# Performance work log

Measured on AMD Instinct MI355X. Metric: run time of the kernel, lower is better.

## Reference

```python
import jax, jax.numpy as jnp
import numpy as np

B, T, D = 64, 512, 256   # batch, time, input feat
H = 256                  # LSTM hidden (features)


def setup_inputs() -> dict:
    key = jax.random.key(0)
    ks = jax.random.split(key, 16)
    s = lambda k, shp, fan: jax.random.normal(k, shp, jnp.float32) / np.sqrt(fan)
    return {
        "x":  jax.random.normal(ks[0], (B, T, D), jnp.float32),
        # LSTM params: fused gates order (i, f, g, o)
        "Wi": s(ks[1], (D, 4 * H), D),
        "Wh": s(ks[2], (H, 4 * H), H),
        "b":  jnp.zeros((4 * H,), jnp.float32),
        # single-head attention (head_dim = H)
        "Wq": s(ks[3], (H, H), H), "bq": jnp.zeros((H,), jnp.float32),
        "Wk": s(ks[4], (H, H), H), "bk": jnp.zeros((H,), jnp.float32),
        "Wv": s(ks[5], (H, H), H), "bv": jnp.zeros((H,), jnp.float32),
        "Wo": s(ks[6], (H, H), H), "bo": jnp.zeros((H,), jnp.float32),
        # MLP head
        "W1": s(ks[7], (H, 32), H), "b1": jnp.zeros((32,), jnp.float32),
        "W2": s(ks[8], (32, 3), 32), "b2": jnp.zeros((3,), jnp.float32),
    }


def _lstm_scan(x, Wi, Wh, b):
    # Precompute input-to-hidden projection for all timesteps (batched GEMM)
    xg = jnp.einsum('btd,dg->btg', x, Wi) + b          # [B,T,4H]
    c0 = jnp.zeros((x.shape[0], Wh.shape[0]), x.dtype)
    h0 = jnp.zeros_like(c0)

    def step(carry, xg_t):
        c, h = carry
        g = xg_t + h @ Wh                               # [B,4H]
        i, f, gg, o = jnp.split(g, 4, axis=-1)          # flax gate order i,f,g,o
        c = jax.nn.sigmoid(f) * c + jax.nn.sigmoid(i) * jnp.tanh(gg)
        h = jax.nn.sigmoid(o) * jnp.tanh(c)
        return (c, h), h

    (_, _), hs = jax.lax.scan(step, (c0, h0), jnp.swapaxes(xg, 0, 1))
    return jnp.swapaxes(hs, 0, 1)                       # [B,T,H]


def reference(x, Wi, Wh, b, Wq, bq, Wk, bk, Wv, bv, Wo, bo, W1, b1, W2, b2):
    h = _lstm_scan(x, Wi, Wh, b)                        # [B,T,H]
    # single-head dot-product attention (self-attention)
    q = h @ Wq + bq
    k = h @ Wk + bk
    v = h @ Wv + bv
    scale = 1.0 / np.sqrt(q.shape[-1]).astype(np.float32)
    scores = jnp.einsum('bqd,bkd->bqk', q * scale, k)   # [B,T,T]
    attn = jax.nn.softmax(scores, axis=-1)
    o = jnp.einsum('bqk,bkd->bqd', attn, v)
    o = o @ Wo + bo                                     # output projection
    # head on first timestep
    z = jax.nn.relu(o[:, 0, :] @ W1 + b1)
    return z @ W2 + b2                                  # [B,3]
```

## Files before the change

### kernel.cpp

```cpp
#include <hip/hip_runtime.h>
#include <hip/hip_bf16.h>


typedef __attribute__((ext_vector_type(8))) short short8;
typedef __attribute__((ext_vector_type(4))) float float4v;

__device__ __forceinline__ unsigned short f2bf(float f) {
  unsigned u = __builtin_bit_cast(unsigned, f);
  return (unsigned short)((u + 0x7fffu + ((u >> 16) & 1u)) >> 16);
}
__device__ __forceinline__ float bf2f(unsigned short h) {
  return __builtin_bit_cast(float, ((unsigned)h) << 16);
}
__device__ __forceinline__ float bcl(unsigned u) {
  return __builtin_bit_cast(float, u << 16);
}
__device__ __forceinline__ float bch(unsigned u) {
  return __builtin_bit_cast(float, u & 0xffff0000u);
}
__device__ __forceinline__ float sigm(float x) { return 1.f / (1.f + __expf(-x)); }
__device__ __forceinline__ float tanh_f(float x) { return 1.f - 2.f / (1.f + __expf(2.f * x)); }

__global__ void prep_x(const float* __restrict__ x, unsigned short* __restrict__ xbf) {
  size_t i = ((size_t)blockIdx.x * 256 + threadIdx.x) * 4;
  float4 v = *(const float4*)&x[i];
  unsigned long long pk = (unsigned long long)f2bf(v.x)
                        | ((unsigned long long)f2bf(v.y) << 16)
                        | ((unsigned long long)f2bf(v.z) << 32)
                        | ((unsigned long long)f2bf(v.w) << 48);
  *(unsigned long long*)&xbf[i] = pk;
}

__global__ void prep_wit(const float* __restrict__ Wi, unsigned short* __restrict__ WiT) {
  size_t i = ((size_t)blockIdx.x * 256 + threadIdx.x) * 4;
  float4 v = *(const float4*)&Wi[i];
  int k = (int)(i >> 10), n = (int)(i & 1023);
  WiT[(size_t)(n + 0) * 256 + k] = f2bf(v.x);
  WiT[(size_t)(n + 1) * 256 + k] = f2bf(v.y);
  WiT[(size_t)(n + 2) * 256 + k] = f2bf(v.z);
  WiT[(size_t)(n + 3) * 256 + k] = f2bf(v.w);
}

__global__ void init_hx(unsigned long long* __restrict__ hx) {
  hx[(size_t)blockIdx.x * 256 + threadIdx.x] = 0xffffffff00000000ULL;
}

#define XKP 40
__global__ __launch_bounds__(256) void xg_gemm(const unsigned short* __restrict__ xbf,
                                               const unsigned short* __restrict__ WiT,
                                               const float* __restrict__ bias,
                                               unsigned short* __restrict__ xg) {
  __shared__ unsigned short As[128 * XKP];
  __shared__ unsigned short Bs[128 * XKP];
  const int tid = threadIdx.x;
  const int n0 = blockIdx.x * 128, m0 = blockIdx.y * 128;
  const int wave = tid >> 6, lane = tid & 63, quad = lane >> 4, l16 = lane & 15;
  const int wm = wave >> 1, wn = wave & 1;

  float4v acc[4][4];
#pragma unroll
  for (int i = 0; i < 4; ++i)
#pragma unroll
    for (int j = 0; j < 4; ++j) acc[i][j] = (float4v){0.f, 0.f, 0.f, 0.f};

  const int rr = tid >> 2, c8 = (tid & 3) * 8;
  for (int k0 = 0; k0 < 256; k0 += 32) {
#pragma unroll
    for (int pp = 0; pp < 2; ++pp) {
      int r = pp * 64 + rr;
      *(uint4*)&As[r * XKP + c8] = *(const uint4*)&xbf[(size_t)(m0 + r) * 256 + k0 + c8];
      *(uint4*)&Bs[r * XKP + c8] = *(const uint4*)&WiT[(size_t)(n0 + r) * 256 + k0 + c8];
    }
    __syncthreads();
#pragma unroll
    for (int mt = 0; mt < 4; ++mt) {
      short8 af = *(const short8*)&As[(wm * 64 + mt * 16 + l16) * XKP + quad * 8];
#pragma unroll
      for (int nt = 0; nt < 4; ++nt) {
        short8 bf = *(const short8*)&Bs[(wn * 64 + nt * 16 + l16) * XKP + quad * 8];
        acc[mt][nt] = __builtin_amdgcn_mfma_f32_16x16x32_bf16(af, bf, acc[mt][nt], 0, 0, 0);
      }
    }
    __syncthreads();
  }
#pragma unroll
  for (int nt = 0; nt < 4; ++nt) {
    int col = n0 + wn * 64 + nt * 16 + l16;
    int gate = col >> 8, ggx = (col >> 4) & 15, ul = col & 15;
    float bv = bias[col];
#pragma unroll
    for (int mt = 0; mt < 4; ++mt) {
#pragma unroll
      for (int r = 0; r < 4; ++r) {
        int row = m0 + wm * 64 + mt * 16 + quad * 4 + r;
        int b = row >> 9, t = row & 511;
        xg[(((size_t)ggx * 64 + b) * 512 + t) * 64 + gate * 16 + ul] =
            f2bf(acc[mt][nt][r] + bv);
      }
    }
  }
}

#define KP2 264
__global__ __launch_bounds__(256) void lstm_scan(const float* __restrict__ Wh,
                                                 const unsigned short* __restrict__ xgbuf,
                                                 unsigned short* __restrict__ hout,
                                                 unsigned long long* __restrict__ hx) {
  __shared__ unsigned short WhS[64 * KP2];
  __shared__ unsigned short hA[16 * KP2];
  __shared__ float preS[16 * 68];
  __shared__ float cS[256];
  const int tid = threadIdx.x;
  const int wg = blockIdx.x, bg = wg >> 4, gg = wg & 15;
  const int wave = tid >> 6, lane = tid & 63, quad = lane >> 4, l16 = lane & 15;

  {
    int uu = tid & 15, kh = tid >> 4;
#pragma unroll
    for (int gt = 0; gt < 4; ++gt)
      for (int kb = 0; kb < 16; ++kb) {
        int k = kb * 16 + kh;
        WhS[(gt * 16 + uu) * KP2 + k] = f2bf(Wh[(size_t)k * 1024 + gt * 256 + gg * 16 + uu]);
      }
  }
  for (int i = tid; i < 16 * KP2; i += 256) hA[i] = 0;
  cS[tid] = 0.f;
  __syncthreads();

  const int b_loc = tid >> 4, u_loc = tid & 15;
  const int bgb = bg * 16 + b_loc;
  const int u_glob = gg * 16 + u_loc;
  const int nrow = wave * 16 + l16;
  const unsigned short* xgp0 = xgbuf + ((size_t)(gg * 64 + bgb) * 512) * 64 + u_loc;

  unsigned short xi = xgp0[0], xf = xgp0[16], xG = xgp0[32], xo = xgp0[48];

  for (int t = 0; t < 512; ++t) {
    float4v acc = (float4v){0.f, 0.f, 0.f, 0.f};
#pragma unroll
    for (int kt = 0; kt < 8; ++kt) {
      short8 af = *(const short8*)&hA[l16 * KP2 + kt * 32 + quad * 8];
      short8 bf = *(const short8*)&WhS[nrow * KP2 + kt * 32 + quad * 8];
      acc = __builtin_amdgcn_mfma_f32_16x16x32_bf16(af, bf, acc, 0, 0, 0);
    }
#pragma unroll
    for (int r = 0; r < 4; ++r)
      preS[(quad * 4 + r) * 68 + wave * 16 + l16] = acc[r];

    int tn = (t < 511) ? t + 1 : t;
    const unsigned short* xgn = xgp0 + (size_t)tn * 64;
    unsigned short nxi = xgn[0], nxf = xgn[16], nxG = xgn[32], nxo = xgn[48];
    __syncthreads();

    float gi = preS[b_loc * 68 + 0 * 16 + u_loc] + bf2f(xi);
    float gf = preS[b_loc * 68 + 1 * 16 + u_loc] + bf2f(xf);
    float gG = preS[b_loc * 68 + 2 * 16 + u_loc] + bf2f(xG);
    float go = preS[b_loc * 68 + 3 * 16 + u_loc] + bf2f(xo);
    float c = sigm(gf) * cS[tid] + sigm(gi) * tanh_f(gG);
    cS[tid] = c;
    float h = sigm(go) * tanh_f(c);
    unsigned hb = (unsigned)f2bf(h);
    hA[b_loc * KP2 + u_glob] = (unsigned short)hb;

    const unsigned tg = (unsigned)t;
    unsigned v1 = __shfl_down((int)hb, 1);
    if ((u_loc & 1) == 0) {
      unsigned d0 = hb | (v1 << 16);
      unsigned long long val = (unsigned long long)d0 | ((unsigned long long)tg << 32);
      unsigned long long* dst =
          hx + (((size_t)(t & 1) * 64 + bgb) * 128 + (u_glob >> 1));
      __hip_atomic_store(dst, val, __ATOMIC_RELAXED, __HIP_MEMORY_SCOPE_AGENT);
      *(unsigned*)&hout[((size_t)bgb * 512 + t) * 256 + u_glob] = d0;
    }

    {
      int b2 = tid >> 4, grp = tid & 15;
      if (grp != gg) {
        const unsigned long long* base =
            hx + (((size_t)(t & 1) * 64 + bg * 16 + b2) * 128 + grp * 8);
        unsigned long long w[8];
        int guard = 0;
        bool ok;
        do {
          ok = true;
#pragma unroll
          for (int i = 0; i < 8; ++i) {
            w[i] = __hip_atomic_load(&base[i], __ATOMIC_RELAXED,
                                     __HIP_MEMORY_SCOPE_AGENT);
            ok &= ((unsigned)(w[i] >> 32) == tg);
          }
        } while (!ok && ++guard < (1 << 20));
        int u0 = grp * 16;
#pragma unroll
        for (int i = 0; i < 8; ++i)
          *(unsigned*)&hA[b2 * KP2 + u0 + 2 * i] = (unsigned)w[i];
      }
    }
    xi = nxi; xf = nxf; xG = nxG; xo = nxo;
    __syncthreads();
  }
}

__global__ __launch_bounds__(256) void attn_qu(const unsigned short* __restrict__ hout,
                                               const float* __restrict__ Wq,
                                               const float* __restrict__ bq,
                                               const float* __restrict__ Wk,
                                               const float* __restrict__ bk,
                                               float* __restrict__ us,
                                               float* __restrict__ cbuf) {
  __shared__ float h0S[256], q0S[256], red[256];
  const int b = blockIdx.x, tid = threadIdx.x;
  h0S[tid] = bf2f(hout[(size_t)b * 512 * 256 + tid]);
  __syncthreads();
  float a = 0.f;
  for (int k = 0; k < 256; ++k) a += h0S[k] * Wq[(size_t)k * 256 + tid];
  q0S[tid] = a + bq[tid];
  __syncthreads();
  red[tid] = q0S[tid] * bk[tid];
  __syncthreads();
  for (int s = 128; s > 0; s >>= 1) {
    if (tid < s) red[tid] += red[tid + s];
    __syncthreads();
  }
  if (tid == 0) cbuf[b] = 0.0625f * red[0];
  float acc = 0.f;
  const float* wr = &Wk[(size_t)tid * 256];
  for (int e = 0; e < 256; e += 4) {
    float4 w = *(const float4*)&wr[e];
    acc += w.x * q0S[e] + w.y * q0S[e + 1] + w.z * q0S[e + 2] + w.w * q0S[e + 3];
  }
  us[b * 256 + tid] = 0.0625f * acc;
}

__global__ __launch_bounds__(256) void attn_sm(const unsigned short* __restrict__ hout,
                                               const float* __restrict__ us,
                                               const float* __restrict__ cbuf,
                                               float* __restrict__ hbar) {
  __shared__ float sS[512], red[256], hb4[4][256];
  const int b = blockIdx.x, tid = threadIdx.x, wave = tid >> 6, lane = tid & 63;
  const size_t hb_base = (size_t)b * 512 * 256;
  const float u0 = us[b * 256 + lane * 4 + 0], u1 = us[b * 256 + lane * 4 + 1];
  const float u2 = us[b * 256 + lane * 4 + 2], u3 = us[b * 256 + lane * 4 + 3];
  const float cbv = cbuf[b];
  for (int i = 0; i < 128; ++i) {
    int t = i * 4 + wave;
    unsigned long long hv = *(const unsigned long long*)&hout[hb_base + (size_t)t * 256 + lane * 4];
    unsigned lo = (unsigned)hv, hi = (unsigned)(hv >> 32);
    float p = u0 * bcl(lo) + u1 * bch(lo) + u2 * bcl(hi) + u3 * bch(hi);
    for (int m = 1; m < 64; m <<= 1) p += __shfl_xor(p, m, 64);
    if (lane == 0) sS[t] = p + cbv;
  }
  __syncthreads();
  red[tid] = fmaxf(sS[tid], sS[tid + 256]);
  __syncthreads();
  for (int s = 128; s > 0; s >>= 1) {
    if (tid < s) red[tid] = fmaxf(red[tid], red[tid + s]);
    __syncthreads();
  }
  float mx = red[0];
  __syncthreads();
  float e0 = __expf(sS[tid] - mx), e1 = __expf(sS[tid + 256] - mx);
  sS[tid] = e0; sS[tid + 256] = e1;
  red[tid] = e0 + e1;
  __syncthreads();
  for (int s = 128; s > 0; s >>= 1) {
    if (tid < s) red[tid] += red[tid + s];
    __syncthreads();
  }
  float inv = 1.f / red[0];
  float a0 = 0.f, a1 = 0.f, a2 = 0.f, a3 = 0.f;
  const int d0 = lane * 4;
  for (int i = 0; i < 128; ++i) {
    int t = wave * 128 + i;
    float w = sS[t];
    unsigned long long hv = *(const unsigned long long*)&hout[hb_base + (size_t)t * 256 + d0];
    unsigned lo = (unsigned)hv, hi = (unsigned)(hv >> 32);
    a0 += w * bcl(lo); a1 += w * bch(lo); a2 += w * bcl(hi); a3 += w * bch(hi);
  }
  hb4[wave][d0] = a0; hb4[wave][d0 + 1] = a1; hb4[wave][d0 + 2] = a2; hb4[wave][d0 + 3] = a3;
  __syncthreads();
  hbar[b * 256 + tid] = (hb4[0][tid] + hb4[1][tid] + hb4[2][tid] + hb4[3][tid]) * inv;
}

__global__ __launch_bounds__(256) void head_k(const float* __restrict__ hbar,
                                              const float* __restrict__ Wv, const float* __restrict__ bv,
                                              const float* __restrict__ Wo, const float* __restrict__ bo,
                                              const float* __restrict__ W1, const float* __restrict__ b1,
                                              const float* __restrict__ W2, const float* __restrict__ b2,
                                              float* __restrict__ out) {
  __shared__ float hS[256], oS[256], o1S[256], zS[32];
  const int b = blockIdx.x, tid = threadIdx.x;
  hS[tid] = hbar[b * 256 + tid];
  __syncthreads();
  float a = 0.f;
  for (int k = 0; k < 256; ++k) a += hS[k] * Wv[(size_t)k * 256 + tid];
  oS[tid] = a + bv[tid];
  __syncthreads();
  a = 0.f;
  for (int k = 0; k < 256; ++k) a += oS[k] * Wo[(size_t)k * 256 + tid];
  o1S[tid] = a + bo[tid];
  __syncthreads();
  if (tid < 32) {
    a = 0.f;
    for (int k = 0; k < 256; ++k) a += o1S[k] * W1[k * 32 + tid];
    zS[tid] = fmaxf(a + b1[tid], 0.f);
  }
  __syncthreads();
  if (tid < 3) {
    a = 0.f;
    for (int j = 0; j < 32; ++j) a += zS[j] * W2[j * 3 + tid];
    out[b * 3 + tid] = a + b2[tid];
  }
}

extern "C" void kernel_launch(void* const* d_in, const int* in_sizes, int n_in,
                              void* d_out, int out_size, void* d_ws, size_t ws_size,
                              hipStream_t stream) {
  const float* x  = (const float*)d_in[0];
  const float* Wi = (const float*)d_in[1];
  const float* Wh = (const float*)d_in[2];
  const float* bG = (const float*)d_in[3];
  const float* Wq = (const float*)d_in[4];
  const float* bq = (const float*)d_in[5];
  const float* Wk = (const float*)d_in[6];
  const float* bk = (const float*)d_in[7];
  const float* Wv = (const float*)d_in[8];
  const float* bv = (const float*)d_in[9];
  const float* Wo = (const float*)d_in[10];
  const float* bo = (const float*)d_in[11];
  const float* W1 = (const float*)d_in[12];
  const float* b1 = (const float*)d_in[13];
  const float* W2 = (const float*)d_in[14];
  const float* b2 = (const float*)d_in[15];
  float* out = (float*)d_out;
  char* ws = (char*)d_ws;

  unsigned short* xg    = (unsigned short*)(ws);
  unsigned short* hout  = (unsigned short*)(ws + 67108864);
  unsigned short* xbf   = (unsigned short*)(ws + 83886080);
  unsigned short* WiT   = (unsigned short*)(ws + 100663296);
  unsigned long long* hx = (unsigned long long*)(ws + 101187584);
  float*          us    = (float*)(ws + 101318656);
  float*          cbuf  = (float*)(ws + 101384192);
  float*          hbar  = (float*)(ws + 101385216);

  prep_x<<<dim3(8192), dim3(256), 0, stream>>>(x, xbf);
  prep_wit<<<dim3(256), dim3(256), 0, stream>>>(Wi, WiT);
  init_hx<<<dim3(64), dim3(256), 0, stream>>>(hx);
  xg_gemm<<<dim3(8, 256), dim3(256), 0, stream>>>(xbf, WiT, bG, xg);
  lstm_scan<<<dim3(64), dim3(256), 0, stream>>>(Wh, xg, hout, hx);
  attn_qu<<<dim3(64), dim3(256), 0, stream>>>(hout, Wq, bq, Wk, bk, us, cbuf);
  attn_sm<<<dim3(64), dim3(256), 0, stream>>>(hout, us, cbuf, hbar);
  head_k<<<dim3(64), dim3(256), 0, stream>>>(hbar, Wv, bv, Wo, bo, W1, b1, W2, b2, out);
}
```

Baseline: 1.406 ms.

## Run LSTM scan one batch row per block with register-resident Wh, fuse kernels

The LSTM recurrence is restructured so each block owns a single batch row and all 1024 gate columns. Most of the bf16 Wh is held as MFMA fragments in registers and the rest in swizzled LDS. This replaces the cross-block atomic flag exchange of h between 16 column-group blocks with plain block-level barriers. The xg layout is changed so each unit's four gates are contiguous. Prep kernels are merged into one, which also pre-permutes Wh. The attention kernels and head are fused into one kernel, and the activations use hardware reciprocals. In exchange, each block now runs a 16-wide MFMA with only one valid batch column, so most of the matrix work is wasted. Register pressure also rises with 48 short8 fragments per lane.

```diff
diff --git a/kernel.cpp b/kernel.cpp
--- a/kernel.cpp
+++ b/kernel.cpp
@@ -18,31 +18,49 @@
 __device__ __forceinline__ float bch(unsigned u) {
   return __builtin_bit_cast(float, u & 0xffff0000u);
 }
-__device__ __forceinline__ float sigm(float x) { return 1.f / (1.f + __expf(-x)); }
-__device__ __forceinline__ float tanh_f(float x) { return 1.f - 2.f / (1.f + __expf(2.f * x)); }
-
-__global__ void prep_x(const float* __restrict__ x, unsigned short* __restrict__ xbf) {
-  size_t i = ((size_t)blockIdx.x * 256 + threadIdx.x) * 4;
-  float4 v = *(const float4*)&x[i];
-  unsigned long long pk = (unsigned long long)f2bf(v.x)
-                        | ((unsigned long long)f2bf(v.y) << 16)
-                        | ((unsigned long long)f2bf(v.z) << 32)
-                        | ((unsigned long long)f2bf(v.w) << 48);
-  *(unsigned long long*)&xbf[i] = pk;
-}
-
-__global__ void prep_wit(const float* __restrict__ Wi, unsigned short* __restrict__ WiT) {
-  size_t i = ((size_t)blockIdx.x * 256 + threadIdx.x) * 4;
-  float4 v = *(const float4*)&Wi[i];
-  int k = (int)(i >> 10), n = (int)(i & 1023);
-  WiT[(size_t)(n + 0) * 256 + k] = f2bf(v.x);
-  WiT[(size_t)(n + 1) * 256 + k] = f2bf(v.y);
-  WiT[(size_t)(n + 2) * 256 + k] = f2bf(v.z);
-  WiT[(size_t)(n + 3) * 256 + k] = f2bf(v.w);
-}
-
-__global__ void init_hx(unsigned long long* __restrict__ hx) {
-  hx[(size_t)blockIdx.x * 256 + threadIdx.x] = 0xffffffff00000000ULL;
+__device__ __forceinline__ float sigm(float x) {
+  return __builtin_amdgcn_rcpf(1.f + __expf(-x));
+}
+__device__ __forceinline__ float tanh_f(float x) {
+  return 1.f - 2.f * __builtin_amdgcn_rcpf(1.f + __expf(2.f * x));
+}
+
+__global__ void prep_all(const float* __restrict__ x,
+                         const float* __restrict__ Wi,
+                         const float* __restrict__ Wh,
+                         unsigned short* __restrict__ xbf,
+                         unsigned short* __restrict__ WiT,
+                         unsigned short* __restrict__ WhP) {
+  const int bid = blockIdx.x, tid = threadIdx.x;
+  if (bid < 8192) {
+    size_t i = ((size_t)bid * 256 + tid) * 4;
+    float4 v = *(const float4*)&x[i];
+    unsigned long long pk = (unsigned long long)f2bf(v.x)
+                          | ((unsigned long long)f2bf(v.y) << 16)
+                          | ((unsigned long long)f2bf(v.z) << 32)
+                          | ((unsigned long long)f2bf(v.w) << 48);
+    *(unsigned long long*)&xbf[i] = pk;
+  } else if (bid < 8448) {
+    size_t i = ((size_t)(bid - 8192) * 256 + tid) * 4;
+    float4 v = *(const float4*)&Wi[i];
+    int k = (int)(i >> 10), n = (int)(i & 1023);
+    WiT[(size_t)(n + 0) * 256 + k] = f2bf(v.x);
+    WiT[(size_t)(n + 1) * 256 + k] = f2bf(v.y);
+    WiT[(size_t)(n + 2) * 256 + k] = f2bf(v.z);
+    WiT[(size_t)(n + 3) * 256 + k] = f2bf(v.w);
+  } else {
+    size_t i0 = ((size_t)(bid - 8448) * 256 + tid) * 4;
+    int row = (int)(i0 >> 8);
+    int colnat = (row & 3) * 256 + (row >> 7) * 32 + ((row >> 4) & 7) * 4 +
+                 ((row >> 2) & 3);
+    unsigned long long pk = 0;
+#pragma unroll
+    for (int j = 0; j < 4; ++j) {
+      int k = (int)((i0 + j) & 255);
+      pk |= (unsigned long long)f2bf(Wh[(size_t)k * 1024 + colnat]) << (16 * j);
+    }
+    *(unsigned long long*)&WhP[i0] = pk;
+  }
 }
 
 #define XKP 40
@@ -86,7 +104,7 @@
 #pragma unroll
   for (int nt = 0; nt < 4; ++nt) {
     int col = n0 + wn * 64 + nt * 16 + l16;
-    int gate = col >> 8, ggx = (col >> 4) & 15, ul = col & 15;
+    int gate = col >> 8, u = col & 255;
     float bv = bias[col];
 #pragma unroll
     for (int mt = 0; mt < 4; ++mt) {
@@ -94,123 +112,106 @@
       for (int r = 0; r < 4; ++r) {
         int row = m0 + wm * 64 + mt * 16 + quad * 4 + r;
         int b = row >> 9, t = row & 511;
-        xg[(((size_t)ggx * 64 + b) * 512 + t) * 64 + gate * 16 + ul] =
-            f2bf(acc[mt][nt][r] + bv);
+        xg[(((size_t)b * 512 + t) * 256 + u) * 4 + gate] = f2bf(acc[mt][nt][r] + bv);
       }
     }
   }
 }
 
-#define KP2 264
-__global__ __launch_bounds__(256) void lstm_scan(const float* __restrict__ Wh,
-                                                 const unsigned short* __restrict__ xgbuf,
-                                                 unsigned short* __restrict__ hout,
-                                                 unsigned long long* __restrict__ hx) {
-  __shared__ unsigned short WhS[64 * KP2];
-  __shared__ unsigned short hA[16 * KP2];
-  __shared__ float preS[16 * 68];
-  __shared__ float cS[256];
+#define SWZ(rowv, off) ((off) ^ (((rowv) & 7) << 4))
+__global__ __launch_bounds__(512, 2) void lstm_scan(
+    const unsigned short* __restrict__ WhP,
+    const unsigned short* __restrict__ xg,
+    unsigned short* __restrict__ hout) {
+  __shared__ unsigned short WhL[16 * 16 * 256];
+  __shared__ unsigned short hA[256];
   const int tid = threadIdx.x;
-  const int wg = blockIdx.x, bg = wg >> 4, gg = wg & 15;
+  const int b = blockIdx.x;
   const int wave = tid >> 6, lane = tid & 63, quad = lane >> 4, l16 = lane & 15;
 
+  short8 frA[6][8];
   {
-    int uu = tid & 15, kh = tid >> 4;
-#pragma unroll
-    for (int gt = 0; gt < 4; ++gt)
-      for (int kb = 0; kb < 16; ++kb) {
-        int k = kb * 16 + kh;
-        WhS[(gt * 16 + uu) * KP2 + k] = f2bf(Wh[(size_t)k * 1024 + gt * 256 + gg * 16 + uu]);
-      }
-  }
-  for (int i = tid; i < 16 * KP2; i += 256) hA[i] = 0;
-  cS[tid] = 0.f;
-  __syncthreads();
-
-  const int b_loc = tid >> 4, u_loc = tid & 15;
-  const int bgb = bg * 16 + b_loc;
-  const int u_glob = gg * 16 + u_loc;
-  const int nrow = wave * 16 + l16;
-  const unsigned short* xgp0 = xgbuf + ((size_t)(gg * 64 + bgb) * 512) * 64 + u_loc;
-
-  unsigned short xi = xgp0[0], xf = xgp0[16], xG = xgp0[32], xo = xgp0[48];
+    const unsigned short* src = WhP + ((size_t)(wave * 128) + l16) * 256 + quad * 8;
+#pragma unroll
+    for (int rt = 0; rt < 6; ++rt)
+#pragma unroll
+      for (int kt = 0; kt < 8; ++kt)
+        frA[rt][kt] = *(const short8*)&src[(size_t)rt * 4096 + kt * 32];
+  }
+  for (int it = 0; it < 16; ++it) {
+    int idx = it * 64 + lane;
+    int r32 = idx >> 5, ch = idx & 31;
+    int tile = wave * 2 + (r32 >> 4), rw = r32 & 15;
+    uint4 v = *(const uint4*)&WhP[((size_t)wave * 128 + 96 + r32) * 256 + ch * 8];
+    *(uint4*)((char*)WhL + tile * 8192 + rw * 512 + SWZ(rw, ch * 16)) = v;
+  }
+  for (int i = tid; i < 256; i += 512) hA[i] = 0;
+  __syncthreads();
+
+  const bool act = (l16 < 8);
+  const int u = wave * 32 + l16 * 4 + quad;
+  const unsigned short* xgp = xg + ((size_t)b * 512 * 256 + u) * 4;
+  unsigned short* houtp = hout + (size_t)b * 512 * 256 + u;
+  float c = 0.f;
+
+  const char* ldsA = (const char*)WhL + (wave * 2) * 8192 + l16 * 512;
+  const char* ldsB = ldsA + 8192;
 
   for (int t = 0; t < 512; ++t) {
-    float4v acc = (float4v){0.f, 0.f, 0.f, 0.f};
+    unsigned long long xv = 0;
+    if (act) xv = *(const unsigned long long*)&xgp[(size_t)t * 1024];
+
+    float4v acc[8];
+#pragma unroll
+    for (int rt = 0; rt < 8; ++rt) acc[rt] = (float4v){0.f, 0.f, 0.f, 0.f};
+
 #pragma unroll
     for (int kt = 0; kt < 8; ++kt) {
-      short8 af = *(const short8*)&hA[l16 * KP2 + kt * 32 + quad * 8];
-      short8 bf = *(const short8*)&WhS[nrow * KP2 + kt * 32 + quad * 8];
-      acc = __builtin_amdgcn_mfma_f32_16x16x32_bf16(af, bf, acc, 0, 0, 0);
-    }
-#pragma unroll
-    for (int r = 0; r < 4; ++r)
-      preS[(quad * 4 + r) * 68 + wave * 16 + l16] = acc[r];
-
-    int tn = (t < 511) ? t + 1 : t;
-    const unsigned short* xgn = xgp0 + (size_t)tn * 64;
-    unsigned short nxi = xgn[0], nxf = xgn[16], nxG = xgn[32], nxo = xgn[48];
-    __syncthreads();
-
-    float gi = preS[b_loc * 68 + 0 * 16 + u_loc] + bf2f(xi);
-    float gf = preS[b_loc * 68 + 1 * 16 + u_loc] + bf2f(xf);
-    float gG = preS[b_loc * 68 + 2 * 16 + u_loc] + bf2f(xG);
-    float go = preS[b_loc * 68 + 3 * 16 + u_loc] + bf2f(xo);
-    float c = sigm(gf) * cS[tid] + sigm(gi) * tanh_f(gG);
-    cS[tid] = c;
-    float h = sigm(go) * tanh_f(c);
-    unsigned hb = (unsigned)f2bf(h);
-    hA[b_loc * KP2 + u_glob] = (unsigned short)hb;
-
-    const unsigned tg = (unsigned)t;
-    unsigned v1 = __shfl_down((int)hb, 1);
-    if ((u_loc & 1) == 0) {
-      unsigned d0 = hb | (v1 << 16);
-      unsigned long long val = (unsigned long long)d0 | ((unsigned long long)tg << 32);
-      unsigned long long* dst =
-          hx + (((size_t)(t & 1) * 64 + bgb) * 128 + (u_glob >> 1));
-      __hip_atomic_store(dst, val, __ATOMIC_RELAXED, __HIP_MEMORY_SCOPE_AGENT);
-      *(unsigned*)&hout[((size_t)bgb * 512 + t) * 256 + u_glob] = d0;
-    }
-
-    {
-      int b2 = tid >> 4, grp = tid & 15;
-      if (grp != gg) {
-        const unsigned long long* base =
-            hx + (((size_t)(t & 1) * 64 + bg * 16 + b2) * 128 + grp * 8);
-        unsigned long long w[8];
-        int guard = 0;
-        bool ok;
-        do {
-          ok = true;
-#pragma unroll
-          for (int i = 0; i < 8; ++i) {
-            w[i] = __hip_atomic_load(&base[i], __ATOMIC_RELAXED,
-                                     __HIP_MEMORY_SCOPE_AGENT);
-            ok &= ((unsigned)(w[i] >> 32) == tg);
-          }
-        } while (!ok && ++guard < (1 << 20));
-        int u0 = grp * 16;
-#pragma unroll
-        for (int i = 0; i < 8; ++i)
-          *(unsigned*)&hA[b2 * KP2 + u0 + 2 * i] = (unsigned)w[i];
-      }
-    }
-    xi = nxi; xf = nxf; xG = nxG; xo = nxo;
-    __syncthreads();
-  }
-}
-
-__global__ __launch_bounds__(256) void attn_qu(const unsigned short* __restrict__ hout,
-                                               const float* __restrict__ Wq,
-                                               const float* __restrict__ bq,
-                                               const float* __restrict__ Wk,
-                                               const float* __restrict__ bk,
-                                               float* __restrict__ us,
-                                               float* __restrict__ cbuf) {
-  __shared__ float h0S[256], q0S[256], red[256];
-  const int b = blockIdx.x, tid = threadIdx.x;
-  h0S[tid] = bf2f(hout[(size_t)b * 512 * 256 + tid]);
+      short8 hb = *(const short8*)((const char*)hA + kt * 64 + quad * 16);
+#pragma unroll
+      for (int rt = 0; rt < 6; ++rt)
+        acc[rt] = __builtin_amdgcn_mfma_f32_16x16x32_bf16(frA[rt][kt], hb, acc[rt], 0, 0, 0);
+      short8 a6 = *(const short8*)(ldsA + SWZ(l16, kt * 64 + quad * 16));
+      acc[6] = __builtin_amdgcn_mfma_f32_16x16x32_bf16(a6, hb, acc[6], 0, 0, 0);
+      short8 a7 = *(const short8*)(ldsB + SWZ(l16, kt * 64 + quad * 16));
+      acc[7] = __builtin_amdgcn_mfma_f32_16x16x32_bf16(a7, hb, acc[7], 0, 0, 0);
+    }
+    __syncthreads();
+
+    if (act) {
+      float4v g4 = acc[0];
+#pragma unroll
+      for (int rt = 1; rt < 8; ++rt)
+        if (l16 == rt) g4 = acc[rt];
+      float gi = g4[0] + bf2f((unsigned short)(xv));
+      float gf = g4[1] + bf2f((unsigned short)(xv >> 16));
+      float gG = g4[2] + bf2f((unsigned short)(xv >> 32));
+      float go = g4[3] + bf2f((unsigned short)(xv >> 48));
+      float cc = sigm(gf) * c + sigm(gi) * tanh_f(gG);
+      c = cc;
+      unsigned short hb16 = f2bf(sigm(go) * tanh_f(cc));
+      hA[u] = hb16;
+      houtp[(size_t)t * 256] = hb16;
+    }
+    __syncthreads();
+  }
+}
+
+__global__ __launch_bounds__(256) void attn_head(
+    const unsigned short* __restrict__ hout,
+    const float* __restrict__ Wq, const float* __restrict__ bq,
+    const float* __restrict__ Wk, const float* __restrict__ bk,
+    const float* __restrict__ Wv, const float* __restrict__ bv,
+    const float* __restrict__ Wo, const float* __restrict__ bo,
+    const float* __restrict__ W1, const float* __restrict__ b1,
+    const float* __restrict__ W2, const float* __restrict__ b2,
+    float* __restrict__ out) {
+  __shared__ float h0S[256], q0S[256], red[256], usS[256], sS[512], hb4[4][256];
+  __shared__ float oS[256], o1S[256], zS[32], cbS;
+  const int b = blockIdx.x, tid = threadIdx.x, wave = tid >> 6, lane = tid & 63;
+  const size_t hb_base = (size_t)b * 512 * 256;
+
+  h0S[tid] = bf2f(hout[hb_base + tid]);
   __syncthreads();
   float a = 0.f;
   for (int k = 0; k < 256; ++k) a += h0S[k] * Wq[(size_t)k * 256 + tid];
@@ -222,26 +223,19 @@
     if (tid < s) red[tid] += red[tid + s];
     __syncthreads();
   }
-  if (tid == 0) cbuf[b] = 0.0625f * red[0];
-  float acc = 0.f;
+  if (tid == 0) cbS = 0.0625f * red[0];
+  float acq = 0.f;
   const float* wr = &Wk[(size_t)tid * 256];
   for (int e = 0; e < 256; e += 4) {
     float4 w = *(const float4*)&wr[e];
-    acc += w.x * q0S[e] + w.y * q0S[e + 1] + w.z * q0S[e + 2] + w.w * q0S[e + 3];
-  }
-  us[b * 256 + tid] = 0.0625f * acc;
-}
-
-__global__ __launch_bounds__(256) void attn_sm(const unsigned short* __restrict__ hout,
-                                               const float* __restrict__ us,
-                                               const float* __restrict__ cbuf,
-                                               float* __restrict__ hbar) {
-  __shared__ float sS[512], red[256], hb4[4][256];
-  const int b = blockIdx.x, tid = threadIdx.x, wave = tid >> 6, lane = tid & 63;
-  const size_t hb_base = (size_t)b * 512 * 256;
-  const float u0 = us[b * 256 + lane * 4 + 0], u1 = us[b * 256 + lane * 4 + 1];
-  const float u2 = us[b * 256 + lane * 4 + 2], u3 = us[b * 256 + lane * 4 + 3];
-  const float cbv = cbuf[b];
+    acq += w.x * q0S[e] + w.y * q0S[e + 1] + w.z * q0S[e + 2] + w.w * q0S[e + 3];
+  }
+  usS[tid] = 0.0625f * acq;
+  __syncthreads();
+
+  const float u0 = usS[lane * 4 + 0], u1 = usS[lane * 4 + 1];
+  const float u2 = usS[lane * 4 + 2], u3 = usS[lane * 4 + 3];
+  const float cbv = cbS;
   for (int i = 0; i < 128; ++i) {
     int t = i * 4 + wave;
     unsigned long long hv = *(const unsigned long long*)&hout[hb_base + (size_t)t * 256 + lane * 4];
@@ -279,21 +273,11 @@
   }
   hb4[wave][d0] = a0; hb4[wave][d0 + 1] = a1; hb4[wave][d0 + 2] = a2; hb4[wave][d0 + 3] = a3;
   __syncthreads();
-  hbar[b * 256 + tid] = (hb4[0][tid] + hb4[1][tid] + hb4[2][tid] + hb4[3][tid]) * inv;
-}
-
-__global__ __launch_bounds__(256) void head_k(const float* __restrict__ hbar,
-                                              const float* __restrict__ Wv, const float* __restrict__ bv,
-                                              const float* __restrict__ Wo, const float* __restrict__ bo,
-                                              const float* __restrict__ W1, const float* __restrict__ b1,
-                                              const float* __restrict__ W2, const float* __restrict__ b2,
-                                              float* __restrict__ out) {
-  __shared__ float hS[256], oS[256], o1S[256], zS[32];
-  const int b = blockIdx.x, tid = threadIdx.x;
-  hS[tid] = hbar[b * 256 + tid];
-  __syncthreads();
-  float a = 0.f;
-  for (int k = 0; k < 256; ++k) a += hS[k] * Wv[(size_t)k * 256 + tid];
+  h0S[tid] = (hb4[0][tid] + hb4[1][tid] + hb4[2][tid] + hb4[3][tid]) * inv;
+  __syncthreads();
+
+  a = 0.f;
+  for (int k = 0; k < 256; ++k) a += h0S[k] * Wv[(size_t)k * 256 + tid];
   oS[tid] = a + bv[tid];
   __syncthreads();
   a = 0.f;
@@ -335,21 +319,15 @@
   float* out = (float*)d_out;
   char* ws = (char*)d_ws;
 
-  unsigned short* xg    = (unsigned short*)(ws);
-  unsigned short* hout  = (unsigned short*)(ws + 67108864);
-  unsigned short* xbf   = (unsigned short*)(ws + 83886080);
-  unsigned short* WiT   = (unsigned short*)(ws + 100663296);
-  unsigned long long* hx = (unsigned long long*)(ws + 101187584);
-  float*          us    = (float*)(ws + 101318656);
-  float*          cbuf  = (float*)(ws + 101384192);
-  float*          hbar  = (float*)(ws + 101385216);
-
-  prep_x<<<dim3(8192), dim3(256), 0, stream>>>(x, xbf);
-  prep_wit<<<dim3(256), dim3(256), 0, stream>>>(Wi, WiT);
-  init_hx<<<dim3(64), dim3(256), 0, stream>>>(hx);
+  unsigned short* xg   = (unsigned short*)(ws);
+  unsigned short* hout = (unsigned short*)(ws + 67108864);
+  unsigned short* xbf  = (unsigned short*)(ws + 83886080);
+  unsigned short* WiT  = (unsigned short*)(ws + 100663296);
+  unsigned short* WhP  = (unsigned short*)(ws + 101187584);
+
+  prep_all<<<dim3(8704), dim3(256), 0, stream>>>(x, Wi, Wh, xbf, WiT, WhP);
   xg_gemm<<<dim3(8, 256), dim3(256), 0, stream>>>(xbf, WiT, bG, xg);
-  lstm_scan<<<dim3(64), dim3(256), 0, stream>>>(Wh, xg, hout, hx);
-  attn_qu<<<dim3(64), dim3(256), 0, stream>>>(hout, Wq, bq, Wk, bk, us, cbuf);
-  attn_sm<<<dim3(64), dim3(256), 0, stream>>>(hout, us, cbuf, hbar);
-  head_k<<<dim3(64), dim3(256), 0, stream>>>(hbar, Wv, bv, Wo, bo, W1, b1, W2, b2, out);
-}
+  lstm_scan<<<dim3(64), dim3(512), 0, stream>>>(WhP, xg, hout);
+  attn_head<<<dim3(64), dim3(256), 0, stream>>>(hout, Wq, bq, Wk, bk, Wv, bv,
+                                                Wo, bo, W1, b1, W2, b2, out);
+}
```

New measurement: 1.352 ms. 1.04x faster.
